# Performance work log

Hardware: AMD Instinct MI355X
Metric: run time of the kernel (lower is better)

## Reference

```python
import jax, jax.numpy as jnp
import numpy as np

EPS = 1e-6
B, N, M, C, H = 4, 2048, 1024, 1024, 16
HD = C // H          # 64
HID = 4 * C          # 4096
SCALE = 1.0 / np.sqrt(HD)


def _ln(x, g, b):
    m = x.mean(-1, keepdims=True)
    v = jnp.mean((x - m) ** 2, -1, keepdims=True)
    return (x - m) * jax.lax.rsqrt(v + EPS) * g + b


def _rot(x):
    # interleaved rotate: (-x2, x1) pairs (rotate_half=False path)
    x1, x2 = x[..., ::2], x[..., 1::2]
    return jnp.stack([-x2, x1], axis=-1).reshape(x.shape)


def _apply_rope(x, emb):
    # emb: [N, 2*HD] = cat(sin, cos); x: [B,H,N,HD]
    sin, cos = jnp.split(emb, 2, axis=-1)
    return x * cos + _rot(x) * sin


def _sdpa(q, k, v):
    s = jnp.einsum('bhqd,bhkd->bhqk', q, k) * SCALE
    a = jax.nn.softmax(s, axis=-1)
    return jnp.einsum('bhqk,bhkd->bhqd', a, v)


def _forward(x, ctx, rope,
             wqkv, sa_qg, sa_qb, sa_kg, sa_kb, sa_wo, sa_bo,
             ca_wq, ca_wk, ca_wv, ca_qg, ca_qb, ca_kg, ca_kb, ca_wo, ca_bo, ca_gate,
             w1g, b1g, w1x, b1x, w2, b2, ls0, ls1, ls2):
    Bx, Nx, Cx = x.shape
    Mx = ctx.shape[1]
    # ---- self attention (fused QKV, qk-norm, RoPE) ----
    qkv = (x @ wqkv).reshape(Bx, Nx, 3, H, HD).transpose(2, 0, 3, 1, 4)  # [3,B,H,N,HD]
    q, k, v = qkv[0], qkv[1], qkv[2]
    q = _ln(q, sa_qg, sa_qb)
    k = _ln(k, sa_kg, sa_kb)
    q = _apply_rope(q, rope)
    k = _apply_rope(k, rope)
    sa = _sdpa(q, k, v).transpose(0, 2, 1, 3).reshape(Bx, Nx, Cx)
    sa = sa @ sa_wo + sa_bo
    x = ls0 * sa + x
    # ---- cross attention (GQA degenerate: n_kv_heads == n_q_heads), gated ----
    q = (x @ ca_wq).reshape(Bx, Nx, H, HD).transpose(0, 2, 1, 3)
    k = (ctx @ ca_wk).reshape(Bx, Mx, H, HD).transpose(0, 2, 1, 3)
    v = (ctx @ ca_wv).reshape(Bx, Mx, H, HD).transpose(0, 2, 1, 3)
    q = _ln(q, ca_qg, ca_qb)
    k = _ln(k, ca_kg, ca_kb)
    q = _apply_rope(q, rope)  # rope on queries only; ctx has its own positions
    ca = _sdpa(q, k, v).transpose(0, 2, 1, 3).reshape(Bx, Nx, Cx)
    ca = (ca @ ca_wo + ca_bo) * jnp.tanh(ca_gate)
    x = ls1 * ca + x
    # ---- SwiGLU FFN ----
    h = jax.nn.silu(x @ w1g + b1g) * (x @ w1x + b1x)
    f = h @ w2 + b2
    x = ls2 * f + x
    return x


def setup_inputs() -> dict:
    key = jax.random.key(0)
    ks = iter(jax.random.split(key, 32))
    rn = lambda shape, s=0.02: (jax.random.normal(next(ks), shape, jnp.float32) * s)
    inp = {
        'x': jax.random.normal(next(ks), (B, N, C), jnp.float32),
        'ctx': jax.random.normal(next(ks), (B, M, C), jnp.float32),
    }
    # rotary table: cat(sin, cos), interleaved-repeated freqs -> [N, 2*HD]
    pos = jnp.arange(N, dtype=jnp.float32)
    inv = 1.0 / (10000.0 ** (jnp.arange(0, HD, 2, dtype=jnp.float32) / HD))
    ang = pos[:, None] * inv[None, :]                      # [N, HD/2]
    sin = jnp.repeat(jnp.sin(ang), 2, axis=-1)
    cos = jnp.repeat(jnp.cos(ang), 2, axis=-1)
    inp['rope'] = jnp.concatenate([sin, cos], axis=-1)
    inp.update(
        wqkv=rn((C, 3 * C)),
        sa_qg=jnp.ones((HD,)), sa_qb=jnp.zeros((HD,)),
        sa_kg=jnp.ones((HD,)), sa_kb=jnp.zeros((HD,)),
        sa_wo=rn((C, C)), sa_bo=jnp.zeros((C,)),
        ca_wq=rn((C, C)), ca_wk=rn((C, C)), ca_wv=rn((C, C)),
        ca_qg=jnp.ones((HD,)), ca_qb=jnp.zeros((HD,)),
        ca_kg=jnp.ones((HD,)), ca_kb=jnp.zeros((HD,)),
        ca_wo=rn((C, C)), ca_bo=jnp.zeros((C,)),
        ca_gate=jnp.full((C,), 0.5, jnp.float32),
        w1g=rn((C, HID)), b1g=jnp.zeros((HID,)),
        w1x=rn((C, HID)), b1x=jnp.zeros((HID,)),
        w2=rn((HID, C)), b2=jnp.zeros((C,)),
        ls0=jnp.full((C,), 1e-5, jnp.float32),
        ls1=jnp.full((C,), 1e-5, jnp.float32),
        ls2=jnp.full((C,), 1e-5, jnp.float32),
    )
    return inp


def reference(x, ctx, rope,
              wqkv, sa_qg, sa_qb, sa_kg, sa_kb, sa_wo, sa_bo,
              ca_wq, ca_wk, ca_wv, ca_qg, ca_qb, ca_kg, ca_kb, ca_wo, ca_bo, ca_gate,
              w1g, b1g, w1x, b1x, w2, b2, ls0, ls1, ls2):
    return _forward(x, ctx, rope,
                    wqkv, sa_qg, sa_qb, sa_kg, sa_kb, sa_wo, sa_bo,
                    ca_wq, ca_wk, ca_wv, ca_qg, ca_qb, ca_kg, ca_kb, ca_wo, ca_bo, ca_gate,
                    w1g, b1g, w1x, b1x, w2, b2, ls0, ls1, ls2)
```

## Files before the change

kernel.cpp:

```cpp
#include <hip/hip_runtime.h>
#include <hip/hip_bf16.h>
#include <math.h>


typedef __attribute__((ext_vector_type(8))) short bf16x8;
typedef __attribute__((ext_vector_type(4))) short s16x4;
typedef __attribute__((ext_vector_type(4))) float f32x4;

#define DEV __device__ __forceinline__

DEV unsigned short f2us(float f) {
  __hip_bfloat16 h = __float2bfloat16(f);
  return __builtin_bit_cast(unsigned short, h);
}

DEV void gload_lds16(const void* g, void* l) {
  __builtin_amdgcn_global_load_lds((const __attribute__((address_space(1))) void*)g,
                                   (__attribute__((address_space(3))) void*)l, 16, 0, 0);
}

#define MFMA_BF16_16x16x32 __builtin_amdgcn_mfma_f32_16x16x32_bf16
#define WAITV0 asm volatile("s_waitcnt vmcnt(0)" ::: "memory")


__global__ __launch_bounds__(256) void cvt_f32_bf16(const float* __restrict__ in,
                                                    __hip_bfloat16* __restrict__ out,
                                                    long n) {
  long i = ((long)blockIdx.x * blockDim.x + threadIdx.x) * 4;
  if (i + 3 < n) {
    float4 v = *(const float4*)(in + i);
    out[i + 0] = __float2bfloat16(v.x);
    out[i + 1] = __float2bfloat16(v.y);
    out[i + 2] = __float2bfloat16(v.z);
    out[i + 3] = __float2bfloat16(v.w);
  }
}

__global__ __launch_bounds__(256) void transpose_cvt(const float* __restrict__ w,
                                                     __hip_bfloat16* __restrict__ wT,
                                                     int K, int N) {
  __shared__ float tile[32][33];
  int n0 = blockIdx.x * 32, k0 = blockIdx.y * 32;
  int tx = threadIdx.x, ty = threadIdx.y;
  #pragma unroll
  for (int i = 0; i < 32; i += 8)
    tile[ty + i][tx] = w[(long)(k0 + ty + i) * N + n0 + tx];
  __syncthreads();
  #pragma unroll
  for (int i = 0; i < 32; i += 8)
    wT[(long)(n0 + ty + i) * K + k0 + tx] = __float2bfloat16(tile[tx][ty + i]);
}

__global__ __launch_bounds__(256) void transpose_cvt_ilv(const float* __restrict__ w,
                                                         __hip_bfloat16* __restrict__ wI,
                                                         int K, int N, int ofs) {
  __shared__ float tile[32][33];
  int n0 = blockIdx.x * 32, k0 = blockIdx.y * 32;
  int tx = threadIdx.x, ty = threadIdx.y;
  #pragma unroll
  for (int i = 0; i < 32; i += 8)
    tile[ty + i][tx] = w[(long)(k0 + ty + i) * N + n0 + tx];
  __syncthreads();
  #pragma unroll
  for (int i = 0; i < 32; i += 8) {
    int j = n0 + ty + i;
    int r = 32 * (j >> 4) + (j & 15) + ofs;
    wI[(long)r * K + k0 + tx] = __float2bfloat16(tile[tx][ty + i]);
  }
}

__global__ __launch_bounds__(256) void transpose_v(const __hip_bfloat16* __restrict__ v,
                                                   long vBatch, long vRow,
                                                   __hip_bfloat16* __restrict__ vt,
                                                   int Nkv) {
  __shared__ unsigned short tile[32][36];
  int bh = blockIdx.z;
  int b = bh >> 4, h = bh & 15;
  int kv0 = blockIdx.x * 32;
  int d0 = blockIdx.y * 32;
  int tx = threadIdx.x, ty = threadIdx.y;
  const __hip_bfloat16* src = v + (long)b * vBatch + h * 64 + d0;
  #pragma unroll
  for (int i = 0; i < 32; i += 8)
    tile[ty + i][tx] = __builtin_bit_cast(unsigned short, src[(long)(kv0 + ty + i) * vRow + tx]);
  __syncthreads();
  unsigned short* dst = (unsigned short*)vt + ((long)bh * (Nkv >> 6) + (kv0 >> 6)) * 4608 + (kv0 & 32) + tx;
  #pragma unroll
  for (int i = 0; i < 32; i += 8)
    dst[(long)(d0 + ty + i) * 72] = tile[tx][ty + i];
}

__global__ __launch_bounds__(256) void ln_rope(__hip_bfloat16* __restrict__ buf,
                                               const float* __restrict__ rope,
                                               const float* __restrict__ g0,
                                               const float* __restrict__ b0,
                                               const float* __restrict__ g1,
                                               const float* __restrict__ b1,
                                               int Rows, int W,
                                               long rowStride, long whichStride,
                                               int ropeMask, long total) {
  int lane = threadIdx.x & 63;
  int wv = threadIdx.x >> 6;
  long id = (long)blockIdx.x * 4 + wv;
  if (id >= total) return;
  int which = (int)(id % W);
  long t = id / W;
  int h = (int)(t & 15); t >>= 4;
  int n = (int)(t % Rows);
  int b = (int)(t / Rows);
  __hip_bfloat16* p = buf + ((long)b * Rows + n) * rowStride + (long)which * whichStride + h * 64 + lane;
  float v = __bfloat162float(*p);
  float s = v;
  #pragma unroll
  for (int m = 32; m; m >>= 1) s += __shfl_xor(s, m);
  float mean = s * (1.f / 64.f);
  float d = v - mean;
  float q = d * d;
  #pragma unroll
  for (int m = 32; m; m >>= 1) q += __shfl_xor(q, m);
  float rstd = rsqrtf(q * (1.f / 64.f) + 1e-6f);
  const float* g = which ? g1 : g0;
  const float* bb = which ? b1 : b0;
  float xn = d * rstd * g[lane] + bb[lane];
  if ((ropeMask >> which) & 1) {
    float partner = __shfl_xor(xn, 1);
    float sn = rope[(long)n * 128 + lane];
    float cs = rope[(long)n * 128 + 64 + lane];
    xn = (lane & 1) ? (xn * cs + partner * sn) : (xn * cs - partner * sn);
  }
  *p = __float2bfloat16(xn);
}

template <int EPI>
DEV void epi_store(long idx, long col, float v,
                   float* __restrict__ out_f, __hip_bfloat16* __restrict__ out_b,
                   const float* __restrict__ bias, const float* __restrict__ scale,
                   const float* __restrict__ gate, const float* __restrict__ resid,
                   const __hip_bfloat16* __restrict__ mulin) {
  if constexpr (EPI == 0) {
    out_b[idx] = __float2bfloat16(v);
  } else if constexpr (EPI == 1) {
    float r = scale[col] * (v + bias[col]) + resid[idx];
    out_f[idx] = r;
    out_b[idx] = __float2bfloat16(r);
  } else if constexpr (EPI == 2) {
    float r = scale[col] * ((v + bias[col]) * tanhf(gate[col])) + resid[idx];
    out_f[idx] = r;
    out_b[idx] = __float2bfloat16(r);
  } else if constexpr (EPI == 3) {
    float z = v + bias[col];
    out_b[idx] = __float2bfloat16(z / (1.f + expf(-z)));
  } else if constexpr (EPI == 4) {
    float z = (v + bias[col]) * __bfloat162float(mulin[idx]);
    out_b[idx] = __float2bfloat16(z);
  } else {
    out_f[idx] = scale[col] * (v + bias[col]) + resid[idx];
  }
}

template <int BM, int EPI>
__global__ __launch_bounds__(512, 2) void gemm2ph(const __hip_bfloat16* __restrict__ A,
                                                  const __hip_bfloat16* __restrict__ Bt,
                                                  int M, int N, int K,
                                                  float* __restrict__ out_f,
                                                  __hip_bfloat16* __restrict__ out_b,
                                                  const float* __restrict__ bias,
                                                  const float* __restrict__ scale,
                                                  const float* __restrict__ gate,
                                                  const float* __restrict__ resid,
                                                  const __hip_bfloat16* __restrict__ mulin) {
  constexpr int MF = BM / 32;
  constexpr int WRS = BM / 2;
  constexpr int AJ = BM * 8 / 512;
  __shared__ __align__(16) unsigned short As[2][BM * 64];
  __shared__ __align__(16) unsigned short Bs[2][256 * 64];

  int t = threadIdx.x;
  int l = t & 63, w = t >> 6;
  int lo = l & 15, hi = l >> 4;
  int wr = w >> 2, wc = w & 3;
  long bm = blockIdx.x, bn = blockIdx.y;
  const __hip_bfloat16* Ab = A + bm * BM * (long)K;
  const __hip_bfloat16* Bb = Bt + bn * 256 * (long)K;
  int nt = K >> 6;

  auto stage = [&](int kt, int buf) {
    long kb = (long)kt * 64;
    #pragma unroll
    for (int j = 0; j < AJ; j++) {
      int q = j * 512 + t;
      int row = q >> 3, c = (q & 7) ^ (row & 7);
      gload_lds16(Ab + (long)row * K + kb + c * 8, &As[buf][q * 8]);
    }
    #pragma unroll
    for (int j = 0; j < 4; j++) {
      int q = j * 512 + t;
      int row = q >> 3, c = (q & 7) ^ (row & 7);
      gload_lds16(Bb + (long)row * K + kb + c * 8, &Bs[buf][q * 8]);
    }
  };

  f32x4 acc[MF][4] = {};

  stage(0, 0);
  WAITV0;
  __builtin_amdgcn_s_barrier();

  for (int kt = 0; kt < nt; ++kt) {
    int cur = kt & 1;
    if (kt + 1 < nt) stage(kt + 1, cur ^ 1);

    #pragma unroll
    for (int ks = 0; ks < 2; ks++) {
      bf16x8 bfrag[4];
      #pragma unroll
      for (int n = 0; n < 4; n++) {
        int rb = wc * 64 + n * 16 + lo;
        bfrag[n] = *(const bf16x8*)&Bs[cur][rb * 64 + (((ks << 2) | hi) ^ (rb & 7)) * 8];
      }
      #pragma unroll
      for (int mg = 0; mg < MF; mg += 4) {
        bf16x8 afrag[4];
        #pragma unroll
        for (int m = 0; m < 4; m++) {
          int ra = wr * WRS + (mg + m) * 16 + lo;
          afrag[m] = *(const bf16x8*)&As[cur][ra * 64 + (((ks << 2) | hi) ^ (ra & 7)) * 8];
        }
        __builtin_amdgcn_s_setprio(1);
        #pragma unroll
        for (int m = 0; m < 4; m++)
          #pragma unroll
          for (int n = 0; n < 4; n++)
            acc[mg + m][n] = MFMA_BF16_16x16x32(afrag[m], bfrag[n], acc[mg + m][n], 0, 0, 0);
        __builtin_amdgcn_s_setprio(0);
      }
    }

    if (kt + 1 < nt) {
      WAITV0;
      __builtin_amdgcn_s_barrier();
    }
  }

  if constexpr (EPI == 6) {
    #pragma unroll
    for (int m = 0; m < MF; m++)
      #pragma unroll
      for (int np = 0; np < 2; np++)
        #pragma unroll
        for (int i = 0; i < 4; i++) {
          long row = bm * BM + wr * WRS + m * 16 + hi * 4 + i;
          long jc = bn * 128 + wc * 32 + np * 16 + lo;
          float g = acc[m][np * 2][i] + bias[jc];
          float xv = acc[m][np * 2 + 1][i] + gate[jc];
          float hv = (g / (1.f + expf(-g))) * xv;
          out_b[row * (long)(N >> 1) + jc] = __float2bfloat16(hv);
        }
  } else {
    #pragma unroll
    for (int m = 0; m < MF; m++)
      #pragma unroll
      for (int n = 0; n < 4; n++)
        #pragma unroll
        for (int i = 0; i < 4; i++) {
          long row = bm * BM + wr * WRS + m * 16 + hi * 4 + i;
          long col = bn * 256 + wc * 64 + n * 16 + lo;
          epi_store<EPI>(row * (long)N + col, col, acc[m][n][i],
                         out_f, out_b, bias, scale, gate, resid, mulin);
        }
  }
}

__global__ __launch_bounds__(256) void attn32(const __hip_bfloat16* __restrict__ qB, long qBatch, long qRow,
                                              const __hip_bfloat16* __restrict__ kB, long kBatch, long kRow,
                                              const __hip_bfloat16* __restrict__ vt,
                                              __hip_bfloat16* __restrict__ out, int Nq, int Nkv) {
  const float SC2 = 0.125f * 1.44269504089f;
  int t = threadIdx.x;
  int l = t & 63, w = t >> 6;
  int lo = l & 15, hi = l >> 4;
  int nQC = Nq >> 7;
  int qc = blockIdx.x % nQC;
  int bh = blockIdx.x / nQC;
  int h = bh & 15, b = bh >> 4;
  int q0 = qc * 128 + w * 32;

  __shared__ unsigned short P_all[4][32 * 72];
  __shared__ unsigned short V_lds[2][64 * 72];
  unsigned short* P = P_all[w];

  bf16x8 qf[2][2];
#pragma unroll
  for (int qs = 0; qs < 2; qs++) {
    const __hip_bfloat16* qp = qB + (long)b * qBatch + (long)(q0 + qs * 16 + lo) * qRow + h * 64 + hi * 8;
    qf[qs][0] = *(const bf16x8*)qp;
    qf[qs][1] = *(const bf16x8*)(qp + 32);
  }

  float mrow[2] = {-INFINITY, -INFINITY};
  float lsum[2] = {0.f, 0.f};
  f32x4 acc[2][4] = {};
  const f32x4 fz = {0.f, 0.f, 0.f, 0.f};

  const __hip_bfloat16* kbase = kB + (long)b * kBatch + h * 64 + hi * 8;
  int nt = Nkv >> 6;
  const char* vtb = (const char*)vt + (long)bh * nt * 9216;

  auto stageV = [&](int tile, unsigned short* dstb) {
    const char* src = vtb + (long)tile * 9216;
    gload_lds16(src + t * 16, &dstb[t * 8]);
    gload_lds16(src + (t + 256) * 16, &dstb[(t + 256) * 8]);
    if (t < 64) gload_lds16(src + (t + 512) * 16, &dstb[(t + 512) * 8]);
  };
  auto loadK = [&](int tile, bf16x8 (&kg)[4][2]) {
#pragma unroll
    for (int g = 0; g < 4; g++) {
      const __hip_bfloat16* kp = kbase + (long)(tile * 64 + g * 16 + lo) * kRow;
      kg[g][0] = *(const bf16x8*)kp;
      kg[g][1] = *(const bf16x8*)(kp + 32);
    }
  };
  auto qkt = [&](bf16x8 (&kg)[4][2], f32x4 (&ST)[2][4]) {
    __builtin_amdgcn_s_setprio(1);
#pragma unroll
    for (int qs = 0; qs < 2; qs++)
#pragma unroll
      for (int g = 0; g < 4; g++) {
        f32x4 s0 = MFMA_BF16_16x16x32(kg[g][0], qf[qs][0], fz, 0, 0, 0);
        ST[qs][g] = MFMA_BF16_16x16x32(kg[g][1], qf[qs][1], s0, 0, 0, 0);
      }
    __builtin_amdgcn_s_setprio(0);
  };
  auto smax = [&](f32x4 (&ST)[2][4]) {
#pragma unroll
    for (int qs = 0; qs < 2; qs++) {
      float mg0 = fmaxf(fmaxf(ST[qs][0][0], ST[qs][0][1]), fmaxf(ST[qs][0][2], ST[qs][0][3]));
      float mg1 = fmaxf(fmaxf(ST[qs][1][0], ST[qs][1][1]), fmaxf(ST[qs][1][2], ST[qs][1][3]));
      float mg2 = fmaxf(fmaxf(ST[qs][2][0], ST[qs][2][1]), fmaxf(ST[qs][2][2], ST[qs][2][3]));
      float mg3 = fmaxf(fmaxf(ST[qs][3][0], ST[qs][3][1]), fmaxf(ST[qs][3][2], ST[qs][3][3]));
      float rm = fmaxf(fmaxf(mg0, mg1), fmaxf(mg2, mg3)) * SC2;
      rm = fmaxf(rm, __shfl_xor(rm, 16));
      rm = fmaxf(rm, __shfl_xor(rm, 32));
      if (!__all(rm <= mrow[qs] + 8.f)) {
        float mn = fmaxf(mrow[qs], rm);
        float scl = exp2f(mrow[qs] - mn);
        mrow[qs] = mn;
        lsum[qs] *= scl;
        float c0 = __shfl(scl, hi * 4 + 0);
        float c1 = __shfl(scl, hi * 4 + 1);
        float c2 = __shfl(scl, hi * 4 + 2);
        float c3 = __shfl(scl, hi * 4 + 3);
#pragma unroll
        for (int tt = 0; tt < 4; tt++) {
          acc[qs][tt][0] *= c0; acc[qs][tt][1] *= c1;
          acc[qs][tt][2] *= c2; acc[qs][tt][3] *= c3;
        }
      }
      float m = mrow[qs];
      float rs = 0.f;
#pragma unroll
      for (int g = 0; g < 4; g++) {
        float p0 = exp2f(fmaf(ST[qs][g][0], SC2, -m));
        float p1 = exp2f(fmaf(ST[qs][g][1], SC2, -m));
        float p2 = exp2f(fmaf(ST[qs][g][2], SC2, -m));
        float p3 = exp2f(fmaf(ST[qs][g][3], SC2, -m));
        rs += (p0 + p1) + (p2 + p3);
        s16x4 pw;
        pw[0] = (short)f2us(p0); pw[1] = (short)f2us(p1);
        pw[2] = (short)f2us(p2); pw[3] = (short)f2us(p3);
        *(s16x4*)&P[(qs * 16 + lo) * 72 + g * 16 + hi * 4] = pw;
      }
      rs += __shfl_xor(rs, 16);
      rs += __shfl_xor(rs, 32);
      lsum[qs] += rs;
    }
  };
  auto pv = [&](const unsigned short* Vb) {
    bf16x8 pf[2][2];
#pragma unroll
    for (int qs = 0; qs < 2; qs++) {
      pf[qs][0] = *(const bf16x8*)&P[(qs * 16 + lo) * 72 + hi * 8];
      pf[qs][1] = *(const bf16x8*)&P[(qs * 16 + lo) * 72 + 32 + hi * 8];
    }
    __builtin_amdgcn_s_setprio(1);
#pragma unroll
    for (int tt = 0; tt < 4; tt++) {
      bf16x8 v0 = *(const bf16x8*)&Vb[(tt * 16 + lo) * 72 + hi * 8];
      bf16x8 v1 = *(const bf16x8*)&Vb[(tt * 16 + lo) * 72 + 32 + hi * 8];
#pragma unroll
      for (int qs = 0; qs < 2; qs++) {
        acc[qs][tt] = MFMA_BF16_16x16x32(pf[qs][0], v0, acc[qs][tt], 0, 0, 0);
        acc[qs][tt] = MFMA_BF16_16x16x32(pf[qs][1], v1, acc[qs][tt], 0, 0, 0);
      }
    }
    __builtin_amdgcn_s_setprio(0);
  };

  bf16x8 kgA[4][2], kgB[4][2];
  stageV(0, V_lds[0]);
  loadK(0, kgA);

  for (int it = 0; it < nt; it += 2) {
    __syncthreads();
    stageV(it + 1, V_lds[1]);
    f32x4 ST0[2][4];
    qkt(kgA, ST0);
    loadK(it + 1, kgB);
    smax(ST0);
    pv(V_lds[0]);

    __syncthreads();
    if (it + 2 < nt) stageV(it + 2, V_lds[0]);
    f32x4 ST1[2][4];
    qkt(kgB, ST1);
    if (it + 2 < nt) loadK(it + 2, kgA);
    smax(ST1);
    pv(V_lds[1]);
  }

#pragma unroll
  for (int qs = 0; qs < 2; qs++) {
    float inv = 1.f / lsum[qs];
    float iv0 = __shfl(inv, hi * 4 + 0);
    float iv1 = __shfl(inv, hi * 4 + 1);
    float iv2 = __shfl(inv, hi * 4 + 2);
    float iv3 = __shfl(inv, hi * 4 + 3);
    float iv[4] = {iv0, iv1, iv2, iv3};
#pragma unroll
    for (int i = 0; i < 4; i++) {
      long row = q0 + qs * 16 + hi * 4 + i;
      __hip_bfloat16* op = out + ((long)b * Nq + row) * 1024 + h * 64 + lo;
#pragma unroll
      for (int tt = 0; tt < 4; tt++) op[tt * 16] = __float2bfloat16(acc[qs][tt][i] * iv[i]);
    }
  }
}


extern "C" void kernel_launch(void* const* d_in, const int* in_sizes, int n_in,
                              void* d_out, int out_size, void* d_ws, size_t ws_size,
                              hipStream_t stream) {
  (void)in_sizes; (void)n_in; (void)out_size; (void)ws_size;

  const float* x      = (const float*)d_in[0];
  const float* ctx    = (const float*)d_in[1];
  const float* rope   = (const float*)d_in[2];
  const float* wqkv   = (const float*)d_in[3];
  const float* sa_qg  = (const float*)d_in[4];
  const float* sa_qb  = (const float*)d_in[5];
  const float* sa_kg  = (const float*)d_in[6];
  const float* sa_kb  = (const float*)d_in[7];
  const float* sa_wo  = (const float*)d_in[8];
  const float* sa_bo  = (const float*)d_in[9];
  const float* ca_wq  = (const float*)d_in[10];
  const float* ca_wk  = (const float*)d_in[11];
  const float* ca_wv  = (const float*)d_in[12];
  const float* ca_qg  = (const float*)d_in[13];
  const float* ca_qb  = (const float*)d_in[14];
  const float* ca_kg  = (const float*)d_in[15];
  const float* ca_kb  = (const float*)d_in[16];
  const float* ca_wo  = (const float*)d_in[17];
  const float* ca_bo  = (const float*)d_in[18];
  const float* ca_gate= (const float*)d_in[19];
  const float* w1g    = (const float*)d_in[20];
  const float* b1g    = (const float*)d_in[21];
  const float* w1x    = (const float*)d_in[22];
  const float* b1x    = (const float*)d_in[23];
  const float* w2     = (const float*)d_in[24];
  const float* b2     = (const float*)d_in[25];
  const float* ls0    = (const float*)d_in[26];
  const float* ls1    = (const float*)d_in[27];
  const float* ls2    = (const float*)d_in[28];

  char* ws = (char*)d_ws;

  const long OFF_WQKVT = 0;
  const long OFF_SAWOT = 6291456;
  const long OFF_CAWQT = 8388608;
  const long OFF_CAWKT = 10485760;
  const long OFF_CAWVT = 12582912;
  const long OFF_CAWOT = 14680064;
  const long OFF_W1I   = 16777216;
  const long OFF_W2T   = 33554432;
  const long OFF_XB    = 41943040;
  const long OFF_QC    = OFF_XB;
  const long OFF_CTXB  = 58720256;
  const long OFF_QKV   = 67108864;
  const long OFF_CAO   = 67108864;
  const long OFF_X2B   = 83886080;
  const long OFF_SG    = 100663296;
  const long OFF_SAO   = 117440512;
  const long OFF_KVC   = 117440512;
  const long OFF_X1    = 134217728;
  const long OFF_X1B   = 167772160;
  const long OFF_CAVT  = OFF_X1B;
  const long OFF_X2    = 184549376;
  const long OFF_SAVT  = OFF_X2;

  auto bfp = [&](long off) { return (__hip_bfloat16*)(ws + off); };
  auto ffp = [&](long off) { return (float*)(ws + off); };

  dim3 tb32(32, 8);
  transpose_cvt<<<dim3(96, 32), tb32, 0, stream>>>(wqkv,  bfp(OFF_WQKVT), 1024, 3072);
  transpose_cvt<<<dim3(32, 32), tb32, 0, stream>>>(sa_wo, bfp(OFF_SAWOT), 1024, 1024);
  transpose_cvt<<<dim3(32, 32), tb32, 0, stream>>>(ca_wq, bfp(OFF_CAWQT), 1024, 1024);
  transpose_cvt<<<dim3(32, 32), tb32, 0, stream>>>(ca_wk, bfp(OFF_CAWKT), 1024, 1024);
  transpose_cvt<<<dim3(32, 32), tb32, 0, stream>>>(ca_wv, bfp(OFF_CAWVT), 1024, 1024);
  transpose_cvt<<<dim3(32, 32), tb32, 0, stream>>>(ca_wo, bfp(OFF_CAWOT), 1024, 1024);
  transpose_cvt_ilv<<<dim3(128, 32), tb32, 0, stream>>>(w1g, bfp(OFF_W1I), 1024, 4096, 0);
  transpose_cvt_ilv<<<dim3(128, 32), tb32, 0, stream>>>(w1x, bfp(OFF_W1I), 1024, 4096, 16);
  transpose_cvt<<<dim3(32, 128), tb32, 0, stream>>>(w2,   bfp(OFF_W2T), 4096, 1024);

  cvt_f32_bf16<<<8192, 256, 0, stream>>>(x,   bfp(OFF_XB),   8388608);
  cvt_f32_bf16<<<4096, 256, 0, stream>>>(ctx, bfp(OFF_CTXB), 4194304);

  gemm2ph<128, 0><<<dim3(64, 12), 512, 0, stream>>>(bfp(OFF_XB), bfp(OFF_WQKVT), 8192, 3072, 1024,
                                                    nullptr, bfp(OFF_QKV), nullptr, nullptr, nullptr, nullptr, nullptr);

  transpose_v<<<dim3(64, 2, 64), tb32, 0, stream>>>(bfp(OFF_QKV) + 2048, (long)2048 * 3072, 3072,
                                                    bfp(OFF_SAVT), 2048);

  ln_rope<<<65536, 256, 0, stream>>>(bfp(OFF_QKV), rope, sa_qg, sa_qb, sa_kg, sa_kb,
                                     2048, 2, 3 * 1024, 1024, 3, (long)4 * 2048 * 16 * 2);

  attn32<<<1024, 256, 0, stream>>>(bfp(OFF_QKV),        (long)2048 * 3072, 3072,
                                   bfp(OFF_QKV) + 1024, (long)2048 * 3072, 3072,
                                   bfp(OFF_SAVT), bfp(OFF_SAO), 2048, 2048);

  gemm2ph<128, 1><<<dim3(64, 4), 512, 0, stream>>>(bfp(OFF_SAO), bfp(OFF_SAWOT), 8192, 1024, 1024,
                                                   ffp(OFF_X1), bfp(OFF_X1B), sa_bo, ls0, nullptr, x, nullptr);

  gemm2ph<128, 0><<<dim3(64, 4), 512, 0, stream>>>(bfp(OFF_X1B), bfp(OFF_CAWQT), 8192, 1024, 1024,
                                                   nullptr, bfp(OFF_QC), nullptr, nullptr, nullptr, nullptr, nullptr);
  gemm2ph<128, 0><<<dim3(32, 8), 512, 0, stream>>>(bfp(OFF_CTXB), bfp(OFF_CAWKT), 4096, 2048, 1024,
                                                   nullptr, bfp(OFF_KVC), nullptr, nullptr, nullptr, nullptr, nullptr);

  transpose_v<<<dim3(32, 2, 64), tb32, 0, stream>>>(bfp(OFF_KVC) + 1024, (long)1024 * 2048, 2048,
                                                    bfp(OFF_CAVT), 1024);

  ln_rope<<<32768, 256, 0, stream>>>(bfp(OFF_QC), rope, ca_qg, ca_qb, ca_qg, ca_qb,
                                     2048, 1, 1024, 0, 1, (long)4 * 2048 * 16);
  ln_rope<<<16384, 256, 0, stream>>>(bfp(OFF_KVC), rope, ca_kg, ca_kb, ca_kg, ca_kb,
                                     1024, 1, 2048, 0, 0, (long)4 * 1024 * 16);

  attn32<<<1024, 256, 0, stream>>>(bfp(OFF_QC), (long)2048 * 1024, 1024,
                                   bfp(OFF_KVC), (long)1024 * 2048, 2048,
                                   bfp(OFF_CAVT), bfp(OFF_CAO), 2048, 1024);

  gemm2ph<128, 2><<<dim3(64, 4), 512, 0, stream>>>(bfp(OFF_CAO), bfp(OFF_CAWOT), 8192, 1024, 1024,
                                                   ffp(OFF_X2), bfp(OFF_X2B), ca_bo, ls1, ca_gate, ffp(OFF_X1), nullptr);

  gemm2ph<256, 6><<<dim3(32, 32), 512, 0, stream>>>(bfp(OFF_X2B), bfp(OFF_W1I), 8192, 8192, 1024,
                                                    nullptr, bfp(OFF_SG), b1g, nullptr, b1x, nullptr, nullptr);

  gemm2ph<128, 5><<<dim3(64, 4), 512, 0, stream>>>(bfp(OFF_SG), bfp(OFF_W2T), 8192, 1024, 4096,
                                                   (float*)d_out, nullptr, b2, ls2, nullptr, ffp(OFF_X2), nullptr);
}
```

Baseline: 878.3 us.

## Run SwiGLU FFN GEMMs in FP8 with fp8 weights and activations

Adds a software float-to-FP8 (e4m3) converter and an FP8 variant of the two-phase GEMM that uses the 16x16x32 fp8 MFMA. The FFN weights are transposed straight to fp8, the cross-attention output projection also writes an fp8 copy of its result, and the SwiGLU GEMM writes its hidden activation in fp8. The aim is to roughly halve operand bytes and use the higher fp8 matrix throughput for the two largest GEMMs. In exchange, precision drops a lot: there is no per-tensor scaling, and the error only stays small because the layer-scale factor on the FFN branch shrinks its contribution.

Measured after the change: 949.7 us. 8.1% more time.

```diff
diff --git a/kernel.cpp b/kernel.cpp
--- a/kernel.cpp
+++ b/kernel.cpp
@@ -14,12 +14,31 @@
   return __builtin_bit_cast(unsigned short, h);
 }
 
+DEV unsigned char f2fp8(float f) {
+  unsigned u = __builtin_bit_cast(unsigned, f);
+  unsigned char s = (unsigned char)((u >> 24) & 0x80u);
+  unsigned a = u & 0x7fffffffu;
+  if (a >= 0x43e00000u) return (unsigned char)(s | 0x7e);
+  if (a < 0x3a000000u) return s;
+  float sc = __builtin_bit_cast(float, a) * 512.0f;
+  unsigned q = (unsigned)(sc + 0.5f);
+  if (q == 0u) return s;
+  if (q < 8u) return (unsigned char)(s | q);
+  if (q < 16u) return (unsigned char)(s | (1u << 3) | (q - 8u));
+  int msb = 31 - __builtin_clz(q);
+  int t = msb - 3;
+  unsigned r = (q + (1u << (t - 1))) >> t;
+  if (r >= 16u) { r >>= 1; t++; }
+  return (unsigned char)(s | ((unsigned)(t + 1) << 3) | (r - 8u));
+}
+
 DEV void gload_lds16(const void* g, void* l) {
   __builtin_amdgcn_global_load_lds((const __attribute__((address_space(1))) void*)g,
                                    (__attribute__((address_space(3))) void*)l, 16, 0, 0);
 }
 
 #define MFMA_BF16_16x16x32 __builtin_amdgcn_mfma_f32_16x16x32_bf16
+#define MFMA_FP8_16x16x32  __builtin_amdgcn_mfma_f32_16x16x32_fp8_fp8
 #define WAITV0 asm volatile("s_waitcnt vmcnt(0)" ::: "memory")
 
 
@@ -51,9 +70,9 @@
     wT[(long)(n0 + ty + i) * K + k0 + tx] = __float2bfloat16(tile[tx][ty + i]);
 }
 
-__global__ __launch_bounds__(256) void transpose_cvt_ilv(const float* __restrict__ w,
-                                                         __hip_bfloat16* __restrict__ wI,
-                                                         int K, int N, int ofs) {
+__global__ __launch_bounds__(256) void transpose_cvt8(const float* __restrict__ w,
+                                                      unsigned char* __restrict__ wT,
+                                                      int K, int N) {
   __shared__ float tile[32][33];
   int n0 = blockIdx.x * 32, k0 = blockIdx.y * 32;
   int tx = threadIdx.x, ty = threadIdx.y;
@@ -62,10 +81,25 @@
     tile[ty + i][tx] = w[(long)(k0 + ty + i) * N + n0 + tx];
   __syncthreads();
   #pragma unroll
+  for (int i = 0; i < 32; i += 8)
+    wT[(long)(n0 + ty + i) * K + k0 + tx] = f2fp8(tile[tx][ty + i]);
+}
+
+__global__ __launch_bounds__(256) void transpose_cvt_ilv8(const float* __restrict__ w,
+                                                          unsigned char* __restrict__ wI,
+                                                          int K, int N, int ofs) {
+  __shared__ float tile[32][33];
+  int n0 = blockIdx.x * 32, k0 = blockIdx.y * 32;
+  int tx = threadIdx.x, ty = threadIdx.y;
+  #pragma unroll
+  for (int i = 0; i < 32; i += 8)
+    tile[ty + i][tx] = w[(long)(k0 + ty + i) * N + n0 + tx];
+  __syncthreads();
+  #pragma unroll
   for (int i = 0; i < 32; i += 8) {
     int j = n0 + ty + i;
     int r = 32 * (j >> 4) + (j & 15) + ofs;
-    wI[(long)r * K + k0 + tx] = __float2bfloat16(tile[tx][ty + i]);
+    wI[(long)r * K + k0 + tx] = f2fp8(tile[tx][ty + i]);
   }
 }
 
@@ -147,12 +181,11 @@
     float r = scale[col] * ((v + bias[col]) * tanhf(gate[col])) + resid[idx];
     out_f[idx] = r;
     out_b[idx] = __float2bfloat16(r);
-  } else if constexpr (EPI == 3) {
-    float z = v + bias[col];
-    out_b[idx] = __float2bfloat16(z / (1.f + expf(-z)));
-  } else if constexpr (EPI == 4) {
-    float z = (v + bias[col]) * __bfloat162float(mulin[idx]);
-    out_b[idx] = __float2bfloat16(z);
+  } else if constexpr (EPI == 7) {
+    float r = scale[col] * ((v + bias[col]) * tanhf(gate[col])) + resid[idx];
+    out_f[idx] = r;
+    out_b[idx] = __float2bfloat16(r);
+    ((unsigned char*)mulin)[idx] = f2fp8(r);
   } else {
     out_f[idx] = scale[col] * (v + bias[col]) + resid[idx];
   }
@@ -242,6 +275,104 @@
     }
   }
 
+  #pragma unroll
+  for (int m = 0; m < MF; m++)
+    #pragma unroll
+    for (int n = 0; n < 4; n++)
+      #pragma unroll
+      for (int i = 0; i < 4; i++) {
+        long row = bm * BM + wr * WRS + m * 16 + hi * 4 + i;
+        long col = bn * 256 + wc * 64 + n * 16 + lo;
+        epi_store<EPI>(row * (long)N + col, col, acc[m][n][i],
+                       out_f, out_b, bias, scale, gate, resid, mulin);
+      }
+}
+
+template <int BM, int EPI>
+__global__ __launch_bounds__(512, 2) void gemm2ph8(const unsigned char* __restrict__ A,
+                                                   const unsigned char* __restrict__ Bt,
+                                                   int M, int N, int K,
+                                                   float* __restrict__ out_f,
+                                                   unsigned char* __restrict__ out_8,
+                                                   const float* __restrict__ bias,
+                                                   const float* __restrict__ scale,
+                                                   const float* __restrict__ gate,
+                                                   const float* __restrict__ resid) {
+  constexpr int MF = BM / 32;
+  constexpr int WRS = BM / 2;
+  constexpr int AJ = BM * 4 / 512;
+  __shared__ __align__(16) unsigned char As[2][BM * 64];
+  __shared__ __align__(16) unsigned char Bs[2][256 * 64];
+
+  int t = threadIdx.x;
+  int l = t & 63, w = t >> 6;
+  int lo = l & 15, hi = l >> 4;
+  int wr = w >> 2, wc = w & 3;
+  long bm = blockIdx.x, bn = blockIdx.y;
+  const unsigned char* Ab = A + bm * BM * (long)K;
+  const unsigned char* Bb = Bt + bn * 256 * (long)K;
+  int nt = K >> 6;
+
+  auto stage = [&](int kt, int buf) {
+    long kb = (long)kt * 64;
+    #pragma unroll
+    for (int j = 0; j < AJ; j++) {
+      int q = j * 512 + t;
+      int row = q >> 2, g = (q & 3) ^ (row & 3);
+      gload_lds16(Ab + (long)row * K + kb + g * 16, &As[buf][q * 16]);
+    }
+    #pragma unroll
+    for (int j = 0; j < 2; j++) {
+      int q = j * 512 + t;
+      int row = q >> 2, g = (q & 3) ^ (row & 3);
+      gload_lds16(Bb + (long)row * K + kb + g * 16, &Bs[buf][q * 16]);
+    }
+  };
+
+  f32x4 acc[MF][4] = {};
+
+  stage(0, 0);
+  WAITV0;
+  __builtin_amdgcn_s_barrier();
+
+  for (int kt = 0; kt < nt; ++kt) {
+    int cur = kt & 1;
+    if (kt + 1 < nt) stage(kt + 1, cur ^ 1);
+
+    #pragma unroll
+    for (int ks = 0; ks < 2; ks++) {
+      int o = (ks << 5) | (hi << 3);
+      int go = o >> 4, rem = o & 15;
+      long long bfrag[4];
+      #pragma unroll
+      for (int n = 0; n < 4; n++) {
+        int rb = wc * 64 + n * 16 + lo;
+        bfrag[n] = *(const long long*)&Bs[cur][rb * 64 + (((go ^ (rb & 3)) << 4) | rem)];
+      }
+      #pragma unroll
+      for (int mg = 0; mg < MF; mg += 4) {
+        long long afrag[4];
+        #pragma unroll
+        for (int m = 0; m < 4; m++) {
+          int ra = wr * WRS + (mg + m) * 16 + lo;
+          afrag[m] = *(const long long*)&As[cur][ra * 64 + (((go ^ (ra & 3)) << 4) | rem)];
+        }
+        __builtin_amdgcn_s_setprio(1);
+        #pragma unroll
+        for (int m = 0; m < 4; m++)
+          #pragma unroll
+          for (int n = 0; n < 4; n++)
+            acc[mg + m][n] = MFMA_FP8_16x16x32(afrag[m], bfrag[n], acc[mg + m][n], 0, 0, 0);
+        __builtin_amdgcn_s_setprio(0);
+      }
+    }
+
+    if (kt + 1 < nt) {
+      WAITV0;
+      __builtin_amdgcn_s_barrier();
+    }
+  }
+
   if constexpr (EPI == 6) {
     #pragma unroll
     for (int m = 0; m < MF; m++)
@@ -254,7 +385,7 @@
           float g = acc[m][np * 2][i] + bias[jc];
           float xv = acc[m][np * 2 + 1][i] + gate[jc];
           float hv = (g / (1.f + expf(-g))) * xv;
-          out_b[row * (long)(N >> 1) + jc] = __float2bfloat16(hv);
+          out_8[row * (long)(N >> 1) + jc] = f2fp8(hv);
         }
   } else {
     #pragma unroll
@@ -265,8 +396,8 @@
         for (int i = 0; i < 4; i++) {
           long row = bm * BM + wr * WRS + m * 16 + hi * 4 + i;
           long col = bn * 256 + wc * 64 + n * 16 + lo;
-          epi_store<EPI>(row * (long)N + col, col, acc[m][n][i],
-                         out_f, out_b, bias, scale, gate, resid, mulin);
+          long idx = row * (long)N + col;
+          out_f[idx] = scale[col] * (acc[m][n][i] + bias[col]) + resid[idx];
         }
   }
 }
@@ -480,16 +611,17 @@
   const long OFF_CAWKT = 10485760;
   const long OFF_CAWVT = 12582912;
   const long OFF_CAWOT = 14680064;
-  const long OFF_W1I   = 16777216;
-  const long OFF_W2T   = 33554432;
+  const long OFF_W1I8  = 16777216;
+  const long OFF_X2B8  = 25165824;
+  const long OFF_W2T8  = 33554432;
   const long OFF_XB    = 41943040;
   const long OFF_QC    = OFF_XB;
   const long OFF_CTXB  = 58720256;
   const long OFF_QKV   = 67108864;
   const long OFF_CAO   = 67108864;
   const long OFF_X2B   = 83886080;
-  const long OFF_SG    = 100663296;
-  const long OFF_SAO   = 117440512;
+  const long OFF_SG8   = 100663296;
+  const long OFF_SAO   = 134217728 - 16777216;
   const long OFF_KVC   = 117440512;
   const long OFF_X1    = 134217728;
   const long OFF_X1B   = 167772160;
@@ -499,6 +631,7 @@
 
   auto bfp = [&](long off) { return (__hip_bfloat16*)(ws + off); };
   auto ffp = [&](long off) { return (float*)(ws + off); };
+  auto cfp = [&](long off) { return (unsigned char*)(ws + off); };
 
   dim3 tb32(32, 8);
   transpose_cvt<<<dim3(96, 32), tb32, 0, stream>>>(wqkv,  bfp(OFF_WQKVT), 1024, 3072);
@@ -507,9 +640,9 @@
   transpose_cvt<<<dim3(32, 32), tb32, 0, stream>>>(ca_wk, bfp(OFF_CAWKT), 1024, 1024);
   transpose_cvt<<<dim3(32, 32), tb32, 0, stream>>>(ca_wv, bfp(OFF_CAWVT), 1024, 1024);
   transpose_cvt<<<dim3(32, 32), tb32, 0, stream>>>(ca_wo, bfp(OFF_CAWOT), 1024, 1024);
-  transpose_cvt_ilv<<<dim3(128, 32), tb32, 0, stream>>>(w1g, bfp(OFF_W1I), 1024, 4096, 0);
-  transpose_cvt_ilv<<<dim3(128, 32), tb32, 0, stream>>>(w1x, bfp(OFF_W1I), 1024, 4096, 16);
-  transpose_cvt<<<dim3(32, 128), tb32, 0, stream>>>(w2,   bfp(OFF_W2T), 4096, 1024);
+  transpose_cvt_ilv8<<<dim3(128, 32), tb32, 0, stream>>>(w1g, cfp(OFF_W1I8), 1024, 4096, 0);
+  transpose_cvt_ilv8<<<dim3(128, 32), tb32, 0, stream>>>(w1x, cfp(OFF_W1I8), 1024, 4096, 16);
+  transpose_cvt8<<<dim3(32, 128), tb32, 0, stream>>>(w2,  cfp(OFF_W2T8), 4096, 1024);
 
   cvt_f32_bf16<<<8192, 256, 0, stream>>>(x,   bfp(OFF_XB),   8388608);
   cvt_f32_bf16<<<4096, 256, 0, stream>>>(ctx, bfp(OFF_CTXB), 4194304);
@@ -547,12 +680,13 @@
                                    bfp(OFF_KVC), (long)1024 * 2048, 2048,
                                    bfp(OFF_CAVT), bfp(OFF_CAO), 2048, 1024);
 
-  gemm2ph<128, 2><<<dim3(64, 4), 512, 0, stream>>>(bfp(OFF_CAO), bfp(OFF_CAWOT), 8192, 1024, 1024,
-                                                   ffp(OFF_X2), bfp(OFF_X2B), ca_bo, ls1, ca_gate, ffp(OFF_X1), nullptr);
-
-  gemm2ph<256, 6><<<dim3(32, 32), 512, 0, stream>>>(bfp(OFF_X2B), bfp(OFF_W1I), 8192, 8192, 1024,
-                                                    nullptr, bfp(OFF_SG), b1g, nullptr, b1x, nullptr, nullptr);
-
-  gemm2ph<128, 5><<<dim3(64, 4), 512, 0, stream>>>(bfp(OFF_SG), bfp(OFF_W2T), 8192, 1024, 4096,
-                                                   (float*)d_out, nullptr, b2, ls2, nullptr, ffp(OFF_X2), nullptr);
-}
+  gemm2ph<128, 7><<<dim3(64, 4), 512, 0, stream>>>(bfp(OFF_CAO), bfp(OFF_CAWOT), 8192, 1024, 1024,
+                                                   ffp(OFF_X2), bfp(OFF_X2B), ca_bo, ls1, ca_gate, ffp(OFF_X1),
+                                                   (const __hip_bfloat16*)cfp(OFF_X2B8));
+
+  gemm2ph8<256, 6><<<dim3(32, 32), 512, 0, stream>>>(cfp(OFF_X2B8), cfp(OFF_W1I8), 8192, 8192, 1024,
+                                                     nullptr, cfp(OFF_SG8), b1g, nullptr, b1x, nullptr);
+
+  gemm2ph8<128, 5><<<dim3(64, 4), 512, 0, stream>>>(cfp(OFF_SG8), cfp(OFF_W2T8), 8192, 1024, 4096,
+                                                    (float*)d_out, nullptr, b2, ls2, nullptr, ffp(OFF_X2));
+}
```
